# Kernel tuning notes

Measured on AMD Instinct MI355X. Metric: run time of the kernel, lower is better.

The kernel has to match this reference:

```python
import jax, jax.numpy as jnp
import numpy as np

N_NODES = 10000
N_EDGES = 640000
HIDDEN = 128
OUT = 10

def setup_inputs() -> dict:
    key = jax.random.key(0)
    k1, k2, k3, k4 = jax.random.split(key, 4)
    x = jax.random.normal(k1, (N_NODES, HIDDEN), dtype=jnp.float32)
    edge_index = jax.random.randint(k2, (2, N_EDGES), 0, N_NODES, dtype=jnp.int64)
    # ClassifierMLP2 params: Linear(2*hidden -> hidden) -> ReLU -> Linear(hidden -> out)
    W1 = jax.random.normal(k3, (2 * HIDDEN, HIDDEN), dtype=jnp.float32) / np.sqrt(2 * HIDDEN)
    b1 = jnp.zeros((HIDDEN,), dtype=jnp.float32)
    W2 = jax.random.normal(k4, (HIDDEN, OUT), dtype=jnp.float32) / np.sqrt(HIDDEN)
    b2 = jnp.zeros((OUT,), dtype=jnp.float32)
    return {"x": x, "edge_index": edge_index, "W1": W1, "b1": b1, "W2": W2, "b2": b2}

def reference(x, edge_index, W1, b1, W2, b2):
    # mix_node_features(..., node_feat_mixing='cat'): gather src/dst node
    # embeddings per edge and concatenate along feature dim -> [E, 2*H]
    src, dst = edge_index[0], edge_index[1]
    edges_x = jnp.concatenate([x[src], x[dst]], axis=-1)  # [E, 2H]
    # ClassifierMLP2 (dropout inactive at inference)
    h = jax.nn.relu(edges_x @ W1 + b1)                    # [E, H]
    return h @ W2 + b2                                    # [E, OUT]
```

## Files before the change

kernel.cpp:

```cpp
#include <hip/hip_runtime.h>


typedef _Float16 f16;
typedef _Float16 f16x8 __attribute__((ext_vector_type(8)));
typedef float    f32x4 __attribute__((ext_vector_type(4)));

#define HID  128
#define TWOH 256
#define OUTD 10

__global__ __launch_bounds__(256) void prep_weights(
    const float* __restrict__ W1,
    const float* __restrict__ W2,
    f16* __restrict__ W1P,
    f16* __restrict__ W2P)
{
    const int slot = blockIdx.x * 256 + threadIdx.x;
    if (slot < 4096) {
        const int lane = slot & 63, i = slot >> 6;
        const int r = lane & 15, g = lane >> 4;
        const int T = i >> 2, st = i & 3;
        const int c = T * 16 + r;
        f16x8 v;
#pragma unroll
        for (int j = 0; j < 8; ++j) {
            const int k = st * 32 + g * 8 + j;
            const float w = (c < HID) ? W1[k * HID + c]
                                      : W1[(HID + k) * HID + (c - HID)];
            v[j] = (f16)w;
        }
        *(f16x8*)(W1P + (long)slot * 8) = v;
    } else if (slot < 4096 + 256) {
        const int s2 = slot - 4096;
        const int lane = s2 & 63, st = s2 >> 6;
        const int r = lane & 15, g = lane >> 4;
        f16x8 v;
#pragma unroll
        for (int j = 0; j < 8; ++j)
            v[j] = (r < OUTD) ? (f16)W2[(st * 32 + g * 8 + j) * OUTD + r] : (f16)0.f;
        *(f16x8*)(W2P + (long)s2 * 8) = v;
    }
}

__global__ __launch_bounds__(256, 6) void node_AB(
    const float* __restrict__ x,
    const f16* __restrict__ W1P,
    const float* __restrict__ b1,
    f16* __restrict__ AB,
    int n_nodes)
{
    const int t = threadIdx.x;
    const int lane = t & 63;
    const int r = lane & 15, g = lane >> 4;
    const int wv = t >> 6;
    const int n0 = (blockIdx.x >> 2) * 16;
    const int T = (blockIdx.x & 3) * 4 + wv;
    const int c = T * 16 + r;

    const int xrow = (n0 + r < n_nodes) ? (n0 + r) : (n_nodes - 1);
    float4 xl[4][2];
#pragma unroll
    for (int st = 0; st < 4; ++st) {
        const float* xp = x + (long)xrow * HID + st * 32 + g * 8;
        xl[st][0] = *(const float4*)xp;
        xl[st][1] = *(const float4*)(xp + 4);
    }

    f16x8 w1f[4];
#pragma unroll
    for (int st = 0; st < 4; ++st)
        w1f[st] = *(const f16x8*)(W1P + ((long)(T * 4 + st) * 64 + lane) * 8);
    const float bias = (c < HID) ? b1[c] : 0.f;

    f32x4 acc = {0, 0, 0, 0};
#pragma unroll
    for (int st = 0; st < 4; ++st) {
        f16x8 a;
        a[0] = (f16)xl[st][0].x; a[1] = (f16)xl[st][0].y;
        a[2] = (f16)xl[st][0].z; a[3] = (f16)xl[st][0].w;
        a[4] = (f16)xl[st][1].x; a[5] = (f16)xl[st][1].y;
        a[6] = (f16)xl[st][1].z; a[7] = (f16)xl[st][1].w;
        acc = __builtin_amdgcn_mfma_f32_16x16x32_f16(a, w1f[st], acc, 0, 0, 0);
    }

#pragma unroll
    for (int q = 0; q < 4; ++q) {
        const int node = n0 + g * 4 + q;
        if (node < n_nodes)
            AB[(long)node * TWOH + c] = (f16)(acc[q] + bias);
    }
}

__global__ __launch_bounds__(256, 6) void edge_mlp(
    const f16* __restrict__ AB,
    const int* __restrict__ ei,
    const f16* __restrict__ W2P,
    const float* __restrict__ b2,
    float* __restrict__ out,
    int n_edges)
{
    const int t = threadIdx.x;
    const int lane = t & 63;
    const int r = lane & 15, g = lane >> 4;
    const int wv = t >> 6;

    const long eb = (long)blockIdx.x * 64 + wv * 16;
    const long e = eb + r;
    const long ec = (e < n_edges) ? e : (n_edges - 1);
    const int sn = ei[ec];
    const int dn = ei[(long)n_edges + ec];

    const f16* pa = AB + ((long)sn * TWOH + g * 8);
    const f16* pb = AB + ((long)dn * TWOH + HID + g * 8);
    f16x8 a0 = *(const f16x8*)pa;
    f16x8 a1 = *(const f16x8*)(pa + 32);
    f16x8 a2 = *(const f16x8*)(pa + 64);
    f16x8 a3 = *(const f16x8*)(pa + 96);
    f16x8 c0 = *(const f16x8*)pb;
    f16x8 c1 = *(const f16x8*)(pb + 32);
    f16x8 c2 = *(const f16x8*)(pb + 64);
    f16x8 c3 = *(const f16x8*)(pb + 96);

    f16x8 w2f[4];
#pragma unroll
    for (int st = 0; st < 4; ++st)
        w2f[st] = *(const f16x8*)(W2P + ((long)st * 64 + lane) * 8);
    const float bj = b2[(r < OUTD) ? r : 0];

    const f16x8 zt = {0, 0, 0, 0, 0, 0, 0, 0};
    f32x4 acc = {0, 0, 0, 0};
    f16x8 s;
    s = __builtin_elementwise_max(a0 + c0, zt);
    acc = __builtin_amdgcn_mfma_f32_16x16x32_f16(s, w2f[0], acc, 0, 0, 0);
    s = __builtin_elementwise_max(a1 + c1, zt);
    acc = __builtin_amdgcn_mfma_f32_16x16x32_f16(s, w2f[1], acc, 0, 0, 0);
    s = __builtin_elementwise_max(a2 + c2, zt);
    acc = __builtin_amdgcn_mfma_f32_16x16x32_f16(s, w2f[2], acc, 0, 0, 0);
    s = __builtin_elementwise_max(a3 + c3, zt);
    acc = __builtin_amdgcn_mfma_f32_16x16x32_f16(s, w2f[3], acc, 0, 0, 0);

    if (r < OUTD) {
#pragma unroll
        for (int q = 0; q < 4; ++q) {
            const long ee = eb + g * 4 + q;
            if (ee < n_edges)
                out[ee * OUTD + r] = acc[q] + bj;
        }
    }
}

extern "C" void kernel_launch(void* const* d_in, const int* in_sizes, int n_in,
                              void* d_out, int out_size, void* d_ws, size_t ws_size,
                              hipStream_t stream) {
    const float* x  = (const float*)d_in[0];
    const int*   ei = (const int*)d_in[1];
    const float* W1 = (const float*)d_in[2];
    const float* b1 = (const float*)d_in[3];
    const float* W2 = (const float*)d_in[4];
    const float* b2 = (const float*)d_in[5];
    float* out = (float*)d_out;

    const int n_nodes = in_sizes[0] / HID;
    const int n_edges = in_sizes[1] / 2;

    f16* AB  = (f16*)d_ws;
    f16* W1P = AB + (long)n_nodes * TWOH;
    f16* W2P = W1P + 4096 * 8;

    prep_weights<<<17, 256, 0, stream>>>(W1, W2, W1P, W2P);

    node_AB<<<((n_nodes + 15) / 16) * 4, 256, 0, stream>>>(x, W1P, b1, AB, n_nodes);

    edge_mlp<<<(n_edges + 63) / 64, 256, 0, stream>>>(AB, ei, W2P, b2, out, n_edges);
}
```

Before: 69.87 us.

## Bucket edges by source node range to improve gather locality

Adds a bucket-scatter pass that groups edges into 25 buckets by source-node range, packing src/dst into 16 bits alongside the original edge id. The edge MLP then runs per bucket so that source-row gathers from the node table hit a smaller working set in cache. Outputs are written back through the stored edge id, which makes the writes scattered. This costs two extra launches plus an atomic scatter pass. It drops edges if a bucket overflows its fixed capacity and assumes node ids fit in 16 bits.

```diff
diff --git a/kernel.cpp b/kernel.cpp
--- a/kernel.cpp
+++ b/kernel.cpp
@@ -8,6 +8,11 @@
 #define HID  128
 #define TWOH 256
 #define OUTD 10
+#define NB   25
+
+__global__ void zero_cnt(int* __restrict__ cnt) {
+    if (threadIdx.x < NB) cnt[threadIdx.x] = 0;
+}
 
 __global__ __launch_bounds__(256) void prep_weights(
     const float* __restrict__ W1,
@@ -91,24 +96,63 @@
     }
 }
 
+__global__ __launch_bounds__(256) void bucket_scatter(
+    const int* __restrict__ ei, int n_edges, int npb, int cap,
+    int* __restrict__ cnt, int2* __restrict__ sorted)
+{
+    __shared__ int lcnt[NB], lbase[NB];
+    const int t = threadIdx.x;
+    if (t < NB) lcnt[t] = 0;
+    __syncthreads();
+
+    const int e = blockIdx.x * 256 + t;
+    const bool v = e < n_edges;
+    int b = 0, pos = 0, src = 0, dst = 0;
+    if (v) {
+        src = ei[e];
+        dst = ei[(long)n_edges + e];
+        b = src / npb; if (b > NB - 1) b = NB - 1;
+        pos = atomicAdd(&lcnt[b], 1);
+    }
+    __syncthreads();
+    if (t < NB)
+        lbase[t] = lcnt[t] ? atomicAdd(&cnt[t], lcnt[t]) : 0;
+    __syncthreads();
+    if (v) {
+        const int idx = lbase[b] + pos;
+        if (idx < cap)
+            sorted[(long)b * cap + idx] = make_int2((src << 16) | dst, e);
+    }
+}
+
 __global__ __launch_bounds__(256, 6) void edge_mlp(
     const f16* __restrict__ AB,
-    const int* __restrict__ ei,
+    const int2* __restrict__ sorted,
+    const int* __restrict__ cnt,
+    int cap,
     const f16* __restrict__ W2P,
     const float* __restrict__ b2,
     float* __restrict__ out,
-    int n_edges)
+    int n_nodes)
 {
     const int t = threadIdx.x;
     const int lane = t & 63;
     const int r = lane & 15, g = lane >> 4;
     const int wv = t >> 6;
 
-    const long eb = (long)blockIdx.x * 64 + wv * 16;
-    const long e = eb + r;
-    const long ec = (e < n_edges) ? e : (n_edges - 1);
-    const int sn = ei[ec];
-    const int dn = ei[(long)n_edges + ec];
+    const int bucket = blockIdx.y;
+    const int n = cnt[bucket];
+    const int off = blockIdx.x * 64 + wv * 16;
+    if (off >= n) return;
+
+    const long sbase = (long)bucket * cap;
+    const int sl = off + r;
+    const int slc = (sl < n) ? sl : (n - 1);
+    const int2 se = sorted[sbase + slc];
+    int sn = se.x >> 16;
+    int dn = se.x & 0xFFFF;
+    if (sn >= n_nodes) sn = n_nodes - 1;
+    if (dn >= n_nodes) dn = n_nodes - 1;
 
     const f16* pa = AB + ((long)sn * TWOH + g * 8);
     const f16* pb = AB + ((long)dn * TWOH + HID + g * 8);
@@ -142,9 +186,11 @@
     if (r < OUTD) {
 #pragma unroll
         for (int q = 0; q < 4; ++q) {
-            const long ee = eb + g * 4 + q;
-            if (ee < n_edges)
-                out[ee * OUTD + r] = acc[q] + bj;
+            const int s2i = off + g * 4 + q;
+            if (s2i < n) {
+                const int eo = sorted[sbase + s2i].y;
+                out[(long)eo * OUTD + r] = acc[q] + bj;
+            }
         }
     }
 }
@@ -163,13 +209,25 @@
     const int n_nodes = in_sizes[0] / HID;
     const int n_edges = in_sizes[1] / 2;
 
-    f16* AB  = (f16*)d_ws;
-    f16* W1P = AB + (long)n_nodes * TWOH;
-    f16* W2P = W1P + 4096 * 8;
+    const int npb = (n_nodes + NB - 1) / NB;
+    int cap = n_edges / NB + n_edges / (NB * 4);
+    cap = (cap + 63) & ~63;
+
+    f16*  AB     = (f16*)d_ws;
+    f16*  W1P    = AB + (long)n_nodes * TWOH;
+    f16*  W2P    = W1P + 4096 * 8;
+    int*  cnt    = (int*)(W2P + 256 * 8);
+    int2* sorted = (int2*)(cnt + 256);
+
+    zero_cnt<<<1, 64, 0, stream>>>(cnt);
 
     prep_weights<<<17, 256, 0, stream>>>(W1, W2, W1P, W2P);
 
+    bucket_scatter<<<(n_edges + 255) / 256, 256, 0, stream>>>(
+        ei, n_edges, npb, cap, cnt, sorted);
+
     node_AB<<<((n_nodes + 15) / 16) * 4, 256, 0, stream>>>(x, W1P, b1, AB, n_nodes);
 
-    edge_mlp<<<(n_edges + 63) / 64, 256, 0, stream>>>(AB, ei, W2P, b2, out, n_edges);
-}
+    dim3 egrid(cap / 64, NB);
+    edge_mlp<<<egrid, 256, 0, stream>>>(AB, sorted, cnt, cap, W2P, b2, out, n_nodes);
+}
```

New measurement: 106.5 us. +52.5%, slower.

## Counting-sort edges by source node before the edge MLP for gather locality

Applied to the files above, without the earlier changes.

Adds a histogram, a single-block prefix scan and an atomic scatter that bucket edges by source node into a packed (src<<16|dst, edge id) array. The edge MLP then reads edges in source order, so gathers of the source half of AB hit cache, and writes outputs back through the original edge id. This adds four kernel launches, atomic traffic and scattered output writes. The 16-bit packing only holds while node counts stay below 65536.

```diff
diff --git a/kernel.cpp b/kernel.cpp
--- a/kernel.cpp
+++ b/kernel.cpp
@@ -8,6 +8,59 @@
 #define HID  128
 #define TWOH 256
 #define OUTD 10
+
+__global__ __launch_bounds__(256) void zero_hist(int* __restrict__ h, int n) {
+    const int i = blockIdx.x * 256 + threadIdx.x;
+    if (i < n) h[i] = 0;
+}
+
+__global__ __launch_bounds__(256) void hist_src(
+    const int* __restrict__ ei, int n_edges, int* __restrict__ hist)
+{
+    const int e = blockIdx.x * 256 + threadIdx.x;
+    if (e < n_edges) atomicAdd(&hist[ei[e]], 1);
+}
+
+__global__ __launch_bounds__(1024) void scan_hist(int* __restrict__ hist, int n)
+{
+    __shared__ int part[1024];
+    const int t = threadIdx.x;
+    const int base = t * 10;
+    int v[10], s = 0;
+#pragma unroll
+    for (int i = 0; i < 10; ++i) {
+        const int idx = base + i;
+        v[i] = (idx < n) ? hist[idx] : 0;
+        s += v[i];
+    }
+    part[t] = s;
+    __syncthreads();
+    for (int off = 1; off < 1024; off <<= 1) {
+        const int x = (t >= off) ? part[t - off] : 0;
+        __syncthreads();
+        part[t] += x;
+        __syncthreads();
+    }
+    int run = (t == 0) ? 0 : part[t - 1];
+#pragma unroll
+    for (int i = 0; i < 10; ++i) {
+        const int idx = base + i;
+        if (idx < n) { const int c = v[i]; hist[idx] = run; run += c; }
+    }
+}
+
+__global__ __launch_bounds__(256) void scatter_src(
+    const int* __restrict__ ei, int n_edges,
+    int* __restrict__ offs, int2* __restrict__ sorted)
+{
+    const int e = blockIdx.x * 256 + threadIdx.x;
+    if (e < n_edges) {
+        const int src = ei[e];
+        const int dst = ei[(long)n_edges + e];
+        const int pos = atomicAdd(&offs[src], 1);
+        sorted[pos] = make_int2((src << 16) | dst, e);
+    }
+}
 
 __global__ __launch_bounds__(256) void prep_weights(
     const float* __restrict__ W1,
@@ -93,7 +146,7 @@
 
 __global__ __launch_bounds__(256, 6) void edge_mlp(
     const f16* __restrict__ AB,
-    const int* __restrict__ ei,
+    const int2* __restrict__ sorted,
     const f16* __restrict__ W2P,
     const float* __restrict__ b2,
     float* __restrict__ out,
@@ -104,11 +157,13 @@
     const int r = lane & 15, g = lane >> 4;
     const int wv = t >> 6;
 
-    const long eb = (long)blockIdx.x * 64 + wv * 16;
-    const long e = eb + r;
-    const long ec = (e < n_edges) ? e : (n_edges - 1);
-    const int sn = ei[ec];
-    const int dn = ei[(long)n_edges + ec];
+    const long slot0 = (long)blockIdx.x * 64 + wv * 16;
+    if (slot0 >= n_edges) return;
+    const long sl = slot0 + r;
+    const long slc = (sl < n_edges) ? sl : (n_edges - 1);
+    const int2 se = sorted[slc];
+    const int sn = se.x >> 16;
+    const int dn = se.x & 0xFFFF;
 
     const f16* pa = AB + ((long)sn * TWOH + g * 8);
     const f16* pb = AB + ((long)dn * TWOH + HID + g * 8);
@@ -142,9 +197,11 @@
     if (r < OUTD) {
 #pragma unroll
         for (int q = 0; q < 4; ++q) {
-            const long ee = eb + g * 4 + q;
-            if (ee < n_edges)
-                out[ee * OUTD + r] = acc[q] + bj;
+            const long s2i = slot0 + g * 4 + q;
+            if (s2i < n_edges) {
+                const int eo = sorted[s2i].y;
+                out[(long)eo * OUTD + r] = acc[q] + bj;
+            }
         }
     }
 }
@@ -163,13 +220,23 @@
     const int n_nodes = in_sizes[0] / HID;
     const int n_edges = in_sizes[1] / 2;
 
-    f16* AB  = (f16*)d_ws;
-    f16* W1P = AB + (long)n_nodes * TWOH;
-    f16* W2P = W1P + 4096 * 8;
+    f16*  AB     = (f16*)d_ws;
+    f16*  W1P    = AB + (long)n_nodes * TWOH;
+    f16*  W2P    = W1P + 4096 * 8;
+    int*  hist   = (int*)(W2P + 256 * 8);
+    int2* sorted = (int2*)(hist + ((n_nodes + 63) & ~63));
+
+    zero_hist<<<(n_nodes + 255) / 256, 256, 0, stream>>>(hist, n_nodes);
 
     prep_weights<<<17, 256, 0, stream>>>(W1, W2, W1P, W2P);
 
+    hist_src<<<(n_edges + 255) / 256, 256, 0, stream>>>(ei, n_edges, hist);
+
+    scan_hist<<<1, 1024, 0, stream>>>(hist, n_nodes);
+
+    scatter_src<<<(n_edges + 255) / 256, 256, 0, stream>>>(ei, n_edges, hist, sorted);
+
     node_AB<<<((n_nodes + 15) / 16) * 4, 256, 0, stream>>>(x, W1P, b1, AB, n_nodes);
 
-    edge_mlp<<<(n_edges + 63) / 64, 256, 0, stream>>>(AB, ei, W2P, b2, out, n_edges);
-}
+    edge_mlp<<<(n_edges + 63) / 64, 256, 0, stream>>>(AB, sorted, W2P, b2, out, n_edges);
+}
```

Result: slower. 150.0 us (+114.7%).
